# Optimization experiments

Measured on AMD Instinct MI355X. Metric: run time of the kernel, lower is better.

## Reference

```python
import jax, jax.numpy as jnp
import numpy as np
from jax.ops import segment_sum, segment_max

N_NODES, N_EDGES, N_GRAPHS = 50000, 800000, 128
IN_C, HID, HEADS, CLIN = 64, 64, 4, 32


def gat_layer(x, W, a_s, a_d, b, src, dst, n):
    # GAT-style attention conv with concatenated heads (PyG GATConv math).
    H, C = a_s.shape
    h = (x @ W).reshape(-1, H, C)                      # [N,H,C]
    es = jnp.einsum('nhc,hc->nh', h, a_s)
    ed = jnp.einsum('nhc,hc->nh', h, a_d)
    e = jax.nn.leaky_relu(es[src] + ed[dst], 0.2)      # [E,H]
    m = segment_max(e, dst, num_segments=n)            # stable softmax over incoming edges
    e = jnp.exp(e - m[dst])
    denom = segment_sum(e, dst, num_segments=n)
    alpha = e / jnp.where(denom[dst] > 0, denom[dst], 1.0)
    out = segment_sum(h[src] * alpha[:, :, None], dst, num_segments=n)  # [N,H,C]
    return out.reshape(-1, H * C) + b


def label_prop(x, src, dst, n, num_layers=2, alpha=0.5):
    # PyG LabelPropagation: sym-normalized diffusion, residual mix, clamp to [0,1].
    deg = segment_sum(jnp.ones((src.shape[0],), x.dtype), dst, num_segments=n)
    dis = jnp.where(deg > 0, 1.0 / jnp.sqrt(jnp.maximum(deg, 1.0)), 0.0)
    norm = (dis[src] * dis[dst])[:, None]
    res = (1.0 - alpha) * x
    out = x
    for _ in range(num_layers):
        out = alpha * segment_sum(out[src] * norm, dst, num_segments=n) + res
        out = jnp.clip(out, 0.0, 1.0)
    return out


def mean_pool(x, batch, n_graphs):
    cnt = segment_sum(jnp.ones((x.shape[0],), x.dtype), batch, num_segments=n_graphs)
    s = segment_sum(x, batch, num_segments=n_graphs)
    return s / jnp.maximum(cnt, 1.0)[:, None]


def setup_inputs() -> dict:
    key = jax.random.key(0)
    ks = iter(jax.random.split(key, 32))
    def p(shape, fan_in):
        return jax.random.normal(next(ks), shape, jnp.float32) / np.sqrt(fan_in)
    d = {}
    d['x'] = jax.random.normal(next(ks), (N_NODES, IN_C), jnp.float32)
    d['edge_index'] = jax.random.randint(next(ks), (2, N_EDGES), 0, N_NODES)
    d['batch'] = jnp.sort(jax.random.randint(next(ks), (N_NODES,), 0, N_GRAPHS))
    d['clinical_data'] = jax.random.normal(next(ks), (N_GRAPHS, CLIN), jnp.float32)
    HC = HEADS * HID
    d['W1'] = p((IN_C, HC), IN_C); d['a1s'] = p((HEADS, HID), HID); d['a1d'] = p((HEADS, HID), HID); d['b1'] = jnp.zeros((HC,), jnp.float32)
    d['W2'] = p((HC, HC), HC); d['a2s'] = p((HEADS, HID), HID); d['a2d'] = p((HEADS, HID), HID); d['b2'] = jnp.zeros((HC,), jnp.float32)
    jk = IN_C + 2 * HC  # 576
    d['pp_w1'] = p((jk, 256), jk); d['pp_b1'] = jnp.zeros((256,), jnp.float32)
    d['pp_w2'] = p((256, 128), 256); d['pp_b2'] = jnp.zeros((128,), jnp.float32)
    d['cl_w1'] = p((CLIN, 64), CLIN); d['cl_b1'] = jnp.zeros((64,), jnp.float32)
    d['cl_w2'] = p((64, 32), 64); d['cl_b2'] = jnp.zeros((32,), jnp.float32)
    d['h_w1'] = p((160, 64), 160); d['h_b1'] = jnp.zeros((64,), jnp.float32)
    d['h_w2'] = p((64, 32), 64); d['h_b2'] = jnp.zeros((32,), jnp.float32)
    d['h_w3'] = p((32, 2), 32); d['h_b3'] = jnp.zeros((2,), jnp.float32)
    return d


def reference(x, edge_index, batch, clinical_data,
              W1, a1s, a1d, b1, W2, a2s, a2d, b2,
              pp_w1, pp_b1, pp_w2, pp_b2,
              cl_w1, cl_b1, cl_w2, cl_b2,
              h_w1, h_b1, h_w2, h_b2, h_w3, h_b3):
    src, dst = edge_index[0], edge_index[1]
    n = x.shape[0]
    h0 = x
    h1 = jax.nn.relu(gat_layer(h0, W1, a1s, a1d, b1, src, dst, n))
    h1 = label_prop(h1, src, dst, n)
    h2 = jax.nn.relu(gat_layer(h1, W2, a2s, a2d, b2, src, dst, n))
    h2 = label_prop(h2, src, dst, n)
    combined = jnp.concatenate([h0, h1, h2], axis=-1)           # [N, 576]
    g = mean_pool(combined, batch, N_GRAPHS)                    # [G, 576]
    v_graph = jax.nn.relu(g @ pp_w1 + pp_b1) @ pp_w2 + pp_b2    # [G, 128] (dropout = eval/no-op)
    v_clin = jax.nn.relu(clinical_data @ cl_w1 + cl_b1) @ cl_w2 + cl_b2  # [G, 32]
    z = jnp.concatenate([v_graph, v_clin], axis=-1)             # [G, 160]
    z = jax.nn.relu(z @ h_w1 + h_b1)
    z = jax.nn.relu(z @ h_w2 + h_b2)
    return z @ h_w3 + h_b3                                      # [G, 2]
```

## Files before the change

kernel.cpp:

```cpp
#include <hip/hip_runtime.h>

#define N_NODES 50000
#define N_EDGES 800000
#define N_GRAPHS 128
#define JK 576
#define CAP 192
#define NSB ((N_NODES + 255) / 256)

typedef __attribute__((ext_vector_type(8))) short bf16x8;
typedef __attribute__((ext_vector_type(4))) float f32x4;

__device__ __forceinline__ unsigned f2_to_bf2(float a, float b) {
    unsigned ua = __float_as_uint(a), ub = __float_as_uint(b);
    ua = (ua + 0x7fffu + ((ua >> 16) & 1u)) >> 16;
    ub = (ub + 0x7fffu + ((ub >> 16) & 1u)) >> 16;
    return ua | (ub << 16);
}
__device__ __forceinline__ uint2 f4_to_bf4(float4 v) {
    return make_uint2(f2_to_bf2(v.x, v.y), f2_to_bf2(v.z, v.w));
}
__device__ __forceinline__ float4 bf4_to_f4(uint2 u) {
    float4 r;
    r.x = __uint_as_float(u.x << 16);
    r.y = __uint_as_float(u.x & 0xffff0000u);
    r.z = __uint_as_float(u.y << 16);
    r.w = __uint_as_float(u.y & 0xffff0000u);
    return r;
}

template<int BN, int KK>
__global__ __launch_bounds__(256)
void mfma_gemm(const unsigned short* __restrict__ Abf, int lda,
               const unsigned short* __restrict__ BT,
               unsigned* __restrict__ Cbf, int ldc,
               int M, const float* __restrict__ bias, int relu,
               int a_off, int b_off, int c_off) {
    __shared__ unsigned short As[64][32];
    __shared__ unsigned short Bs[BN][32];
    const int t = threadIdx.x;
    const int wav = t >> 6, lane = t & 63;
    const int quad = lane >> 4, l15 = lane & 15;
    const int m0 = blockIdx.x * 64;
    const int head = blockIdx.y;
    Abf += (size_t)head * a_off;
    BT  += (size_t)head * b_off;
    const float* bptr = bias ? bias + (size_t)head * c_off : nullptr;
    unsigned* cbf = Cbf + (((size_t)head * c_off) >> 1);

    f32x4 acc[BN / 16];
#pragma unroll
    for (int i = 0; i < BN / 16; i++) acc[i] = (f32x4){0.f, 0.f, 0.f, 0.f};

    const int arow = t >> 2, aseg = t & 3;
    for (int k0 = 0; k0 < KK; k0 += 32) {
        uint4 av = make_uint4(0, 0, 0, 0);
        int gm = m0 + arow;
        if (gm < M) av = *(const uint4*)&Abf[(size_t)gm * lda + k0 + aseg * 8];
        uint4 bv[BN == 256 ? 4 : 1];
        if (BN == 256) {
            const unsigned short* srcb = &BT[(size_t)t * KK + k0];
#pragma unroll
            for (int j = 0; j < 4; j++) bv[j] = *(const uint4*)&srcb[j * 8];
        } else {
            bv[0] = *(const uint4*)&BT[(size_t)arow * KK + k0 + aseg * 8];
        }
        __syncthreads();
        *(uint4*)&As[arow][aseg * 8] = av;
        if (BN == 256) {
#pragma unroll
            for (int j = 0; j < 4; j++) *(uint4*)&Bs[t][j * 8] = bv[j];
        } else {
            *(uint4*)&Bs[arow][aseg * 8] = bv[0];
        }
        __syncthreads();
        bf16x8 afrag = *(const bf16x8*)&As[wav * 16 + l15][quad * 8];
#pragma unroll
        for (int nt = 0; nt < BN / 16; nt++) {
            bf16x8 bfrag = *(const bf16x8*)&Bs[nt * 16 + l15][quad * 8];
            acc[nt] = __builtin_amdgcn_mfma_f32_16x16x32_bf16(afrag, bfrag, acc[nt], 0, 0, 0);
        }
    }
    int rbase = m0 + wav * 16 + quad * 4;
#pragma unroll
    for (int nt = 0; nt < BN / 16; nt++) {
        int col = nt * 16 + l15;
        float bb = bptr ? bptr[col] : 0.f;
#pragma unroll
        for (int r = 0; r < 4; r++) {
            int row = rbase + r;
            float v = acc[nt][r] + bb;
            if (relu) v = fmaxf(v, 0.f);
            float vp = __shfl_xor(v, 1);
            if (row < M && !(l15 & 1))
                cbf[((size_t)row * ldc + col) >> 1] = f2_to_bf2(v, vp);
        }
    }
}

__global__ void deg_kernel(const int* __restrict__ dst, int* __restrict__ deg) {
    int t = blockIdx.x * blockDim.x + threadIdx.x;
    if (t < N_EDGES) atomicAdd(&deg[dst[t]], 1);
}
#define S1 50000
#define S2 100000
#define S3 100256
#define S4 101280
#define S5 117664
#define S6 183200
#define S7 1783200
__global__ void prep_misc(const int* __restrict__ deg, float* __restrict__ dis,
                          const int* __restrict__ batch, int* __restrict__ gstart,
                          const float* __restrict__ W1, const float* __restrict__ a1s,
                          const float* __restrict__ a1d, float* __restrict__ wes1,
                          float* __restrict__ wed1,
                          const float* __restrict__ W2, const float* __restrict__ a2s,
                          const float* __restrict__ a2d, float* __restrict__ wes2,
                          float* __restrict__ wed2,
                          unsigned short* __restrict__ W1T, unsigned short* __restrict__ W2T,
                          const float* __restrict__ x, unsigned* __restrict__ xbf) {
    int i = blockIdx.x * blockDim.x + threadIdx.x;
    if (i >= S7) return;
    if (i >= S6) {
        int j = i - S6;
        float2 v = *(const float2*)&x[(size_t)j * 2];
        xbf[j] = f2_to_bf2(v.x, v.y);
    } else if (i >= S5) {
        int t2 = i - S5;
        int n = t2 >> 8, c = t2 & 255;
        unsigned u = __float_as_uint(W2[(size_t)c * 256 + n]);
        u = (u + 0x7fffu + ((u >> 16) & 1u)) >> 16;
        W2T[t2] = (unsigned short)u;
    } else if (i >= S4) {
        int t2 = i - S4;
        int n = t2 >> 6, c = t2 & 63;
        unsigned u = __float_as_uint(W1[(size_t)c * 256 + n]);
        u = (u + 0x7fffu + ((u >> 16) & 1u)) >> 16;
        W1T[t2] = (unsigned short)u;
    } else if (i >= S3) {
        int t2 = i - S3;
        int c = t2 >> 2, h = t2 & 3;
        float se = 0.f, sd = 0.f;
        for (int j = 0; j < 64; j++) {
            float w = W2[(size_t)c * 256 + h * 64 + j];
            se += w * a2s[h * 64 + j];
            sd += w * a2d[h * 64 + j];
        }
        wes2[c * 4 + h] = se;
        wed2[c * 4 + h] = sd;
    } else if (i >= S2) {
        int t2 = i - S2;
        int c = t2 >> 2, h = t2 & 3;
        float se = 0.f, sd = 0.f;
        for (int j = 0; j < 64; j++) {
            float w = W1[(size_t)c * 256 + h * 64 + j];
            se += w * a1s[h * 64 + j];
            sd += w * a1d[h * 64 + j];
        }
        wes1[c * 4 + h] = se;
        wed1[c * 4 + h] = sd;
    } else if (i >= S1) {
        int n = i - S1;
        int b = batch[n];
        int prev = (n == 0) ? -1 : batch[n - 1];
        for (int g = prev + 1; g <= b; g++) gstart[g] = n;
        if (n == N_NODES - 1)
            for (int g = b + 1; g <= N_GRAPHS; g++) gstart[g] = N_NODES;
    } else {
        int d = deg[i];
        dis[i] = d > 0 ? rsqrtf((float)d) : 0.f;
    }
}
__global__ __launch_bounds__(256) void scan_bsum(const int* __restrict__ deg,
                                                 int* __restrict__ bsum) {
    __shared__ int sd[256];
    int n = blockIdx.x * 256 + threadIdx.x;
    sd[threadIdx.x] = (n < N_NODES) ? deg[n] : 0;
    __syncthreads();
    for (int o = 128; o > 0; o >>= 1) {
        if (threadIdx.x < o) sd[threadIdx.x] += sd[threadIdx.x + o];
        __syncthreads();
    }
    if (threadIdx.x == 0) bsum[blockIdx.x] = sd[0];
}
__global__ __launch_bounds__(256) void scan_bpre(const int* __restrict__ bsum,
                                                 int* __restrict__ bpre,
                                                 int* __restrict__ off_last) {
    __shared__ int sd[256];
    int t = threadIdx.x;
    int v = (t < NSB) ? bsum[t] : 0;
    sd[t] = v;
    __syncthreads();
    for (int o = 1; o < 256; o <<= 1) {
        int u = (t >= o) ? sd[t - o] : 0;
        __syncthreads();
        sd[t] += u;
        __syncthreads();
    }
    if (t < NSB) bpre[t] = sd[t] - v;
    if (t == 255) *off_last = sd[255];
}
__global__ __launch_bounds__(256) void scan_off(const int* __restrict__ deg,
                                                const int* __restrict__ bpre,
                                                int* __restrict__ off) {
    __shared__ int sd[256];
    int n = blockIdx.x * 256 + threadIdx.x;
    int t = threadIdx.x;
    int v = (n < N_NODES) ? deg[n] : 0;
    sd[t] = v;
    __syncthreads();
    for (int o = 1; o < 256; o <<= 1) {
        int u = (t >= o) ? sd[t - o] : 0;
        __syncthreads();
        sd[t] += u;
        __syncthreads();
    }
    if (n < N_NODES) off[n] = bpre[blockIdx.x] + sd[t] - v;
}
__global__ void csr_fill(const int* __restrict__ src, const int* __restrict__ dst,
                         const int* __restrict__ off, int* __restrict__ cursor,
                         int* __restrict__ csr_src) {
    int e = blockIdx.x * blockDim.x + threadIdx.x;
    if (e >= N_EDGES) return;
    int s = src[e], d = dst[e];
    int pos = off[d] + atomicAdd(&cursor[d], 1);
    csr_src[pos] = s;
}

__global__ void esed_x(const float* __restrict__ X, const float* __restrict__ wes,
                       const float* __restrict__ wed, float* __restrict__ es,
                       float* __restrict__ ed) {
    int gid = blockIdx.x * blockDim.x + threadIdx.x;
    int n = gid >> 6, lane = threadIdx.x & 63;
    if (n >= N_NODES) return;
    float xv = X[(size_t)n * 64 + lane];
    float4 a = *(const float4*)&wes[lane * 4];
    float4 b = *(const float4*)&wed[lane * 4];
    float4 ps = make_float4(xv * a.x, xv * a.y, xv * a.z, xv * a.w);
    float4 pd = make_float4(xv * b.x, xv * b.y, xv * b.z, xv * b.w);
#pragma unroll
    for (int o = 1; o < 64; o <<= 1) {
        ps.x += __shfl_xor(ps.x, o); ps.y += __shfl_xor(ps.y, o);
        ps.z += __shfl_xor(ps.z, o); ps.w += __shfl_xor(ps.w, o);
        pd.x += __shfl_xor(pd.x, o); pd.y += __shfl_xor(pd.y, o);
        pd.z += __shfl_xor(pd.z, o); pd.w += __shfl_xor(pd.w, o);
    }
    if (lane == 0) {
        *(float4*)&es[n * 4] = ps;
        *(float4*)&ed[n * 4] = pd;
    }
}

__global__ void esed_h(const unsigned* __restrict__ Hbf, const float* __restrict__ wes,
                       const float* __restrict__ wed, float* __restrict__ es,
                       float* __restrict__ ed) {
    int gid = blockIdx.x * blockDim.x + threadIdx.x;
    int n = gid >> 6, lane = threadIdx.x & 63;
    if (n >= N_NODES) return;
    float4 xv = bf4_to_f4(*(const uint2*)&Hbf[(size_t)n * 128 + lane * 2]);
    float xs[4] = {xv.x, xv.y, xv.z, xv.w};
    float4 ps = make_float4(0.f, 0.f, 0.f, 0.f);
    float4 pd = make_float4(0.f, 0.f, 0.f, 0.f);
#pragma unroll
    for (int r = 0; r < 4; r++) {
        int c = lane * 4 + r;
        float4 a = *(const float4*)&wes[c * 4];
        float4 b = *(const float4*)&wed[c * 4];
        ps.x += xs[r] * a.x; ps.y += xs[r] * a.y; ps.z += xs[r] * a.z; ps.w += xs[r] * a.w;
        pd.x += xs[r] * b.x; pd.y += xs[r] * b.y; pd.z += xs[r] * b.z; pd.w += xs[r] * b.w;
    }
#pragma unroll
    for (int o = 1; o < 64; o <<= 1) {
        ps.x += __shfl_xor(ps.x, o); ps.y += __shfl_xor(ps.y, o);
        ps.z += __shfl_xor(ps.z, o); ps.w += __shfl_xor(ps.w, o);
        pd.x += __shfl_xor(pd.x, o); pd.y += __shfl_xor(pd.y, o);
        pd.z += __shfl_xor(pd.z, o); pd.w += __shfl_xor(pd.w, o);
    }
    if (lane == 0) {
        *(float4*)&es[n * 4] = ps;
        *(float4*)&ed[n * 4] = pd;
    }
}

__global__ __launch_bounds__(256)
void gat1_fused(const int* __restrict__ off, const int* __restrict__ csr_src,
                const float* __restrict__ es, const float* __restrict__ ed,
                const unsigned* __restrict__ xbf, unsigned* __restrict__ aggx_bf,
                float* __restrict__ alpha_fb) {
    __shared__ float elds[4][CAP * 4];
    __shared__ int   sidx[4][CAP];
    int wav = threadIdx.x >> 6, lane = threadIdx.x & 63;
    int n = blockIdx.x * 4 + wav;
    bool active = n < N_NODES;
    int p0 = 0, p1 = 0;
    float4 ed4 = make_float4(0.f, 0.f, 0.f, 0.f);
    if (active) { p0 = off[n]; p1 = off[n + 1]; ed4 = *(const float4*)&ed[n * 4]; }
    float4 sum = make_float4(0.f, 0.f, 0.f, 0.f);
    for (int p = p0 + lane; p < p1; p += 64) {
        int s = csr_src[p];
        float4 e4 = *(const float4*)&es[s * 4];
        e4.x += ed4.x; e4.y += ed4.y; e4.z += ed4.z; e4.w += ed4.w;
        e4.x = e4.x > 0.f ? e4.x : 0.2f * e4.x;
        e4.y = e4.y > 0.f ? e4.y : 0.2f * e4.y;
        e4.z = e4.z > 0.f ? e4.z : 0.2f * e4.z;
        e4.w = e4.w > 0.f ? e4.w : 0.2f * e4.w;
        e4.x = __expf(e4.x); e4.y = __expf(e4.y); e4.z = __expf(e4.z); e4.w = __expf(e4.w);
        int q = p - p0;
        if (q < CAP) { *(float4*)&elds[wav][q * 4] = e4; sidx[wav][q] = s; }
        else         *(float4*)&alpha_fb[(size_t)p * 4] = e4;
        sum.x += e4.x; sum.y += e4.y; sum.z += e4.z; sum.w += e4.w;
    }
#pragma unroll
    for (int o = 1; o < 64; o <<= 1) {
        sum.x += __shfl_xor(sum.x, o); sum.y += __shfl_xor(sum.y, o);
        sum.z += __shfl_xor(sum.z, o); sum.w += __shfl_xor(sum.w, o);
    }
    float4 rs;
    rs.x = sum.x > 0.f ? 1.f / sum.x : 0.f;
    rs.y = sum.y > 0.f ? 1.f / sum.y : 0.f;
    rs.z = sum.z > 0.f ? 1.f / sum.z : 0.f;
    rs.w = sum.w > 0.f ? 1.f / sum.w : 0.f;
    if (!active) return;
    int eg = lane >> 4, l15 = lane & 15;
    int deg = p1 - p0;
    float4 a0 = make_float4(0.f, 0.f, 0.f, 0.f);
    float4 a1 = a0, a2 = a0, a3 = a0;
    auto fetch = [&](int qq, float4& e4, float4& xv) {
        e4 = make_float4(0.f, 0.f, 0.f, 0.f);
        xv = e4;
        if (qq < deg) {
            int s;
            if (qq < CAP) { s = sidx[wav][qq]; e4 = *(const float4*)&elds[wav][qq * 4]; }
            else { s = csr_src[p0 + qq]; e4 = *(const float4*)&alpha_fb[(size_t)(p0 + qq) * 4]; }
            xv = bf4_to_f4(*(const uint2*)&xbf[(size_t)s * 32 + l15 * 2]);
        }
    };
    int q = eg;
    float4 eA, xA, eB, xB, eC, xC;
    fetch(q, eA, xA);
    fetch(q + 4, eB, xB);
    fetch(q + 8, eC, xC);
    while (q < deg) {
        float4 eD, xD;
        fetch(q + 12, eD, xD);
        a0.x += eA.x * xA.x; a0.y += eA.x * xA.y; a0.z += eA.x * xA.z; a0.w += eA.x * xA.w;
        a1.x += eA.y * xA.x; a1.y += eA.y * xA.y; a1.z += eA.y * xA.z; a1.w += eA.y * xA.w;
        a2.x += eA.z * xA.x; a2.y += eA.z * xA.y; a2.z += eA.z * xA.z; a2.w += eA.z * xA.w;
        a3.x += eA.w * xA.x; a3.y += eA.w * xA.y; a3.z += eA.w * xA.z; a3.w += eA.w * xA.w;
        eA = eB; xA = xB; eB = eC; xB = xC; eC = eD; xC = xD;
        q += 4;
    }
#pragma unroll
    for (int o = 16; o < 64; o <<= 1) {
        a0.x += __shfl_xor(a0.x, o); a0.y += __shfl_xor(a0.y, o);
        a0.z += __shfl_xor(a0.z, o); a0.w += __shfl_xor(a0.w, o);
        a1.x += __shfl_xor(a1.x, o); a1.y += __shfl_xor(a1.y, o);
        a1.z += __shfl_xor(a1.z, o); a1.w += __shfl_xor(a1.w, o);
        a2.x += __shfl_xor(a2.x, o); a2.y += __shfl_xor(a2.y, o);
        a2.z += __shfl_xor(a2.z, o); a2.w += __shfl_xor(a2.w, o);
        a3.x += __shfl_xor(a3.x, o); a3.y += __shfl_xor(a3.y, o);
        a3.z += __shfl_xor(a3.z, o); a3.w += __shfl_xor(a3.w, o);
    }
    if (eg == 0) {
        a0.x *= rs.x; a0.y *= rs.x; a0.z *= rs.x; a0.w *= rs.x;
        a1.x *= rs.y; a1.y *= rs.y; a1.z *= rs.y; a1.w *= rs.y;
        a2.x *= rs.z; a2.y *= rs.z; a2.z *= rs.z; a2.w *= rs.z;
        a3.x *= rs.w; a3.y *= rs.w; a3.z *= rs.w; a3.w *= rs.w;
        size_t b = (size_t)n * 128 + l15 * 2;
        *(uint2*)&aggx_bf[b +  0] = f4_to_bf4(a0);
        *(uint2*)&aggx_bf[b + 32] = f4_to_bf4(a1);
        *(uint2*)&aggx_bf[b + 64] = f4_to_bf4(a2);
        *(uint2*)&aggx_bf[b + 96] = f4_to_bf4(a3);
    }
}

__global__ __launch_bounds__(256)
void gat2_fused(const int* __restrict__ off, const int* __restrict__ csr_src,
                const float* __restrict__ es, const float* __restrict__ ed,
                const unsigned* __restrict__ H2bf, const float* __restrict__ bias,
                unsigned* __restrict__ outbf, float* __restrict__ alpha_fb) {
    __shared__ float elds[4][CAP * 4];
    __shared__ int   sidx[4][CAP];
    int wav = threadIdx.x >> 6, lane = threadIdx.x & 63;
    int n = blockIdx.x * 4 + wav;
    bool active = n < N_NODES;
    int p0 = 0, p1 = 0;
    float4 ed4 = make_float4(0.f, 0.f, 0.f, 0.f);
    if (active) { p0 = off[n]; p1 = off[n + 1]; ed4 = *(const float4*)&ed[n * 4]; }
    float4 sum = make_float4(0.f, 0.f, 0.f, 0.f);
    for (int p = p0 + lane; p < p1; p += 64) {
        int s = csr_src[p];
        float4 e4 = *(const float4*)&es[s * 4];
        e4.x += ed4.x; e4.y += ed4.y; e4.z += ed4.z; e4.w += ed4.w;
        e4.x = e4.x > 0.f ? e4.x : 0.2f * e4.x;
        e4.y = e4.y > 0.f ? e4.y : 0.2f * e4.y;
        e4.z = e4.z > 0.f ? e4.z : 0.2f * e4.z;
        e4.w = e4.w > 0.f ? e4.w : 0.2f * e4.w;
        e4.x = __expf(e4.x); e4.y = __expf(e4.y); e4.z = __expf(e4.z); e4.w = __expf(e4.w);
        int q = p - p0;
        if (q < CAP) { *(float4*)&elds[wav][q * 4] = e4; sidx[wav][q] = s; }
        else         *(float4*)&alpha_fb[(size_t)p * 4] = e4;
        sum.x += e4.x; sum.y += e4.y; sum.z += e4.z; sum.w += e4.w;
    }
#pragma unroll
    for (int o = 1; o < 64; o <<= 1) {
        sum.x += __shfl_xor(sum.x, o); sum.y += __shfl_xor(sum.y, o);
        sum.z += __shfl_xor(sum.z, o); sum.w += __shfl_xor(sum.w, o);
    }
    if (!active) return;
    int half = lane >> 5, l = lane & 31;
    int hh = l >> 3;
    float sh = (hh == 0) ? sum.x : (hh == 1) ? sum.y : (hh == 2) ? sum.z : sum.w;
    float rsh = sh > 0.f ? 1.f / sh : 0.f;
    int deg = p1 - p0;
    float acc[8];
#pragma unroll
    for (int j = 0; j < 8; j++) acc[j] = 0.f;
    auto fetch = [&](int qq, float& al, uint4& rr) {
        al = 0.f;
        rr = make_uint4(0, 0, 0, 0);
        if (qq < deg) {
            int s;
            if (qq < CAP) { s = sidx[wav][qq]; al = elds[wav][qq * 4 + hh]; }
            else { s = csr_src[p0 + qq]; al = alpha_fb[(size_t)(p0 + qq) * 4 + hh]; }
            rr = *(const uint4*)&H2bf[(size_t)s * 128 + l * 4];
        }
    };
    int q = half;
    float aA, aB, aC;
    uint4 rA, rB, rC;
    fetch(q, aA, rA);
    fetch(q + 2, aB, rB);
    fetch(q + 4, aC, rC);
    while (q < deg) {
        float aD; uint4 rD;
        fetch(q + 6, aD, rD);
        float4 f0 = bf4_to_f4(make_uint2(rA.x, rA.y));
        float4 f1 = bf4_to_f4(make_uint2(rA.z, rA.w));
        acc[0] += aA * f0.x; acc[1] += aA * f0.y; acc[2] += aA * f0.z; acc[3] += aA * f0.w;
        acc[4] += aA * f1.x; acc[5] += aA * f1.y; acc[6] += aA * f1.z; acc[7] += aA * f1.w;
        aA = aB; rA = rB; aB = aC; rB = rC; aC = aD; rC = rD;
        q += 2;
    }
#pragma unroll
    for (int j = 0; j < 8; j++) acc[j] += __shfl_xor(acc[j], 32);
    if (half == 0) {
        float4 b0 = *(const float4*)&bias[l * 8];
        float4 b1 = *(const float4*)&bias[l * 8 + 4];
        float4 o0, o1;
        o0.x = fmaxf(acc[0] * rsh + b0.x, 0.f);
        o0.y = fmaxf(acc[1] * rsh + b0.y, 0.f);
        o0.z = fmaxf(acc[2] * rsh + b0.z, 0.f);
        o0.w = fmaxf(acc[3] * rsh + b0.w, 0.f);
        o1.x = fmaxf(acc[4] * rsh + b1.x, 0.f);
        o1.y = fmaxf(acc[5] * rsh + b1.y, 0.f);
        o1.z = fmaxf(acc[6] * rsh + b1.z, 0.f);
        o1.w = fmaxf(acc[7] * rsh + b1.w, 0.f);
        uint2 w0 = f4_to_bf4(o0), w1 = f4_to_bf4(o1);
        uint4 w = make_uint4(w0.x, w0.y, w1.x, w1.y);
        *(uint4*)&outbf[(size_t)n * 128 + l * 4] = w;
    }
}

__global__ __launch_bounds__(256)
void lp_csr(const int* __restrict__ off, const int* __restrict__ csr_src,
            const float* __restrict__ dis, const unsigned* __restrict__ in_bf,
            const unsigned* __restrict__ res_bf, unsigned* __restrict__ out_bf) {
    __shared__ int   widx[4][CAP];
    __shared__ float wwt[4][CAP];
    int wav = threadIdx.x >> 6, lane = threadIdx.x & 63;
    int n = blockIdx.x * 4 + wav;
    if (n >= N_NODES) return;
    int p0 = off[n], p1 = off[n + 1];
    int deg = p1 - p0;
    float disd = dis[n];
    for (int q = lane; q < deg && q < CAP; q += 64) {
        int s = csr_src[p0 + q];
        widx[wav][q] = s;
        wwt[wav][q] = dis[s] * disd;
    }
    int half = lane >> 5, l = lane & 31;
    float acc[8];
#pragma unroll
    for (int j = 0; j < 8; j++) acc[j] = 0.f;
    auto fetch = [&](int qq, float& nw, uint4& rr) {
        nw = 0.f;
        rr = make_uint4(0, 0, 0, 0);
        if (qq < deg) {
            int s;
            if (qq < CAP) { s = widx[wav][qq]; nw = wwt[wav][qq]; }
            else { s = csr_src[p0 + qq]; nw = dis[s] * disd; }
            rr = *(const uint4*)&in_bf[(size_t)s * 128 + l * 4];
        }
    };
    int q = half;
    float nA, nB, nC;
    uint4 rA, rB, rC;
    fetch(q, nA, rA);
    fetch(q + 2, nB, rB);
    fetch(q + 4, nC, rC);
    while (q < deg) {
        float nD; uint4 rD;
        fetch(q + 6, nD, rD);
        float4 f0 = bf4_to_f4(make_uint2(rA.x, rA.y));
        float4 f1 = bf4_to_f4(make_uint2(rA.z, rA.w));
        acc[0] += nA * f0.x; acc[1] += nA * f0.y; acc[2] += nA * f0.z; acc[3] += nA * f0.w;
        acc[4] += nA * f1.x; acc[5] += nA * f1.y; acc[6] += nA * f1.z; acc[7] += nA * f1.w;
        nA = nB; rA = rB; nB = nC; rB = rC; nC = nD; rC = rD;
        q += 2;
    }
#pragma unroll
    for (int j = 0; j < 8; j++) acc[j] += __shfl_xor(acc[j], 32);
    if (half == 0) {
        uint4 rr = *(const uint4*)&res_bf[(size_t)n * 128 + l * 4];
        float4 r0 = bf4_to_f4(make_uint2(rr.x, rr.y));
        float4 r1 = bf4_to_f4(make_uint2(rr.z, rr.w));
        float4 o0, o1;
        o0.x = fminf(fmaxf(0.5f * acc[0] + 0.5f * r0.x, 0.f), 1.f);
        o0.y = fminf(fmaxf(0.5f * acc[1] + 0.5f * r0.y, 0.f), 1.f);
        o0.z = fminf(fmaxf(0.5f * acc[2] + 0.5f * r0.z, 0.f), 1.f);
        o0.w = fminf(fmaxf(0.5f * acc[3] + 0.5f * r0.w, 0.f), 1.f);
        o1.x = fminf(fmaxf(0.5f * acc[4] + 0.5f * r1.x, 0.f), 1.f);
        o1.y = fminf(fmaxf(0.5f * acc[5] + 0.5f * r1.y, 0.f), 1.f);
        o1.z = fminf(fmaxf(0.5f * acc[6] + 0.5f * r1.z, 0.f), 1.f);
        o1.w = fminf(fmaxf(0.5f * acc[7] + 0.5f * r1.w, 0.f), 1.f);
        uint2 w0 = f4_to_bf4(o0), w1 = f4_to_bf4(o1);
        uint4 w = make_uint4(w0.x, w0.y, w1.x, w1.y);
        *(uint4*)&out_bf[(size_t)n * 128 + l * 4] = w;
    }
}

__global__ void pool_partial(const float* __restrict__ buf, const int* __restrict__ gstart,
                             float* __restrict__ psum, int C, int colOff) {
    int g = blockIdx.x, q = blockIdx.y;
    int n0 = gstart[g], n1 = gstart[g + 1];
    int len = n1 - n0;
    int ns = n0 + (len * q) / 4, ne = n0 + (len * (q + 1)) / 4;
    int cp = threadIdx.x % C;
    int np = threadIdx.x / C;
    int NP = 256 / C;
    float s = 0.f;
    for (int n = ns + np; n < ne; n += NP) s += buf[(size_t)n * C + cp];
    atomicAdd(&psum[g * JK + colOff + cp], s);
}
__global__ void pool_bf(const unsigned* __restrict__ buf, const int* __restrict__ gstart,
                        float* __restrict__ psum, int colOff) {
    int g = blockIdx.x, q = blockIdx.y;
    int n0 = gstart[g], n1 = gstart[g + 1];
    int len = n1 - n0;
    int ns = n0 + (len * q) / 4, ne = n0 + (len * (q + 1)) / 4;
    int cp = threadIdx.x & 127;
    int np = threadIdx.x >> 7;
    float s0 = 0.f, s1 = 0.f;
    for (int n = ns + np; n < ne; n += 2) {
        unsigned u = buf[(size_t)n * 128 + cp];
        s0 += __uint_as_float(u << 16);
        s1 += __uint_as_float(u & 0xffff0000u);
    }
    atomicAdd(&psum[g * JK + colOff + cp * 2 + 0], s0);
    atomicAdd(&psum[g * JK + colOff + cp * 2 + 1], s1);
}
__global__ void gmean_kernel(const float* __restrict__ psum, const int* __restrict__ gstart,
                             float* __restrict__ g) {
    int i = blockIdx.x * blockDim.x + threadIdx.x;
    if (i >= N_GRAPHS * JK) return;
    int gi = i / JK;
    int len = gstart[gi + 1] - gstart[gi];
    g[i] = psum[i] / (float)(len > 1 ? len : 1);
}

__global__ __launch_bounds__(64)
void head_d1(const float* __restrict__ gbuf, const float* __restrict__ W,
             const float* __restrict__ bias, float* __restrict__ out) {
    __shared__ float zin[JK];
    int g = blockIdx.y, mc = blockIdx.x, lane = threadIdx.x;
    for (int k = lane; k < JK; k += 64) zin[k] = gbuf[g * JK + k];
    __syncthreads();
    int m = mc * 64 + lane;
    float acc = bias[m];
#pragma unroll 8
    for (int k = 0; k < JK; k++) acc += zin[k] * W[k * 256 + m];
    out[g * 256 + m] = fmaxf(acc, 0.f);
}

__global__ __launch_bounds__(256)
void head_rest(const float* __restrict__ t1, const float* __restrict__ clin,
               const float* __restrict__ pp_w2, const float* __restrict__ pp_b2,
               const float* __restrict__ cl_w1, const float* __restrict__ cl_b1,
               const float* __restrict__ cl_w2, const float* __restrict__ cl_b2,
               const float* __restrict__ h_w1, const float* __restrict__ h_b1,
               const float* __restrict__ h_w2, const float* __restrict__ h_b2,
               const float* __restrict__ h_w3, const float* __restrict__ h_b3,
               float* __restrict__ out) {
    __shared__ float z1[256];
    __shared__ float zcl[32];
    __shared__ float zc[64];
    __shared__ float z[160];
    __shared__ float z3[64];
    __shared__ float z4[32];
    __shared__ float part[128];
    int g = blockIdx.x, t = threadIdx.x;
    z1[t] = t1[g * 256 + t];
    if (t < 32) zcl[t] = clin[g * 32 + t];
    __syncthreads();
    int m = t & 127, half = t >> 7;
    {
        float acc = 0.f;
        int k0 = half * 128;
#pragma unroll 8
        for (int k = k0; k < k0 + 128; k++) acc += z1[k] * pp_w2[k * 128 + m];
        if (half) part[m] = acc;
        __syncthreads();
        if (!half) z[m] = acc + part[m] + pp_b2[m];
    }
    if (t < 64) {
        float acc = cl_b1[t];
#pragma unroll
        for (int k = 0; k < 32; k++) acc += zcl[k] * cl_w1[k * 64 + t];
        zc[t] = fmaxf(acc, 0.f);
    }
    __syncthreads();
    if (t < 32) {
        float acc = cl_b2[t];
#pragma unroll
        for (int k = 0; k < 64; k++) acc += zc[k] * cl_w2[k * 32 + t];
        z[128 + t] = acc;
    }
    __syncthreads();
    if (t < 64) {
        float acc = h_b1[t];
#pragma unroll 8
        for (int k = 0; k < 160; k++) acc += z[k] * h_w1[k * 64 + t];
        z3[t] = fmaxf(acc, 0.f);
    }
    __syncthreads();
    if (t < 32) {
        float acc = h_b2[t];
#pragma unroll
        for (int k = 0; k < 64; k++) acc += z3[k] * h_w2[k * 32 + t];
        z4[t] = fmaxf(acc, 0.f);
    }
    __syncthreads();
    if (t < 2) {
        float acc = h_b3[t];
#pragma unroll
        for (int k = 0; k < 32; k++) acc += z4[k] * h_w3[k * 2 + t];
        out[g * 2 + t] = acc;
    }
}

extern "C" void kernel_launch(void* const* d_in, const int* in_sizes, int n_in,
                              void* d_out, int out_size, void* d_ws, size_t ws_size,
                              hipStream_t stream) {
    const float* x     = (const float*)d_in[0];
    const int*   ei    = (const int*)d_in[1];
    const int*   batch = (const int*)d_in[2];
    const float* clin  = (const float*)d_in[3];
    const float* W1  = (const float*)d_in[4];
    const float* a1s = (const float*)d_in[5];
    const float* a1d = (const float*)d_in[6];
    const float* b1  = (const float*)d_in[7];
    const float* W2  = (const float*)d_in[8];
    const float* a2s = (const float*)d_in[9];
    const float* a2d = (const float*)d_in[10];
    const float* b2  = (const float*)d_in[11];
    const float* pp_w1 = (const float*)d_in[12];
    const float* pp_b1 = (const float*)d_in[13];
    const float* pp_w2 = (const float*)d_in[14];
    const float* pp_b2 = (const float*)d_in[15];
    const float* cl_w1 = (const float*)d_in[16];
    const float* cl_b1 = (const float*)d_in[17];
    const float* cl_w2 = (const float*)d_in[18];
    const float* cl_b2 = (const float*)d_in[19];
    const float* h_w1  = (const float*)d_in[20];
    const float* h_b1  = (const float*)d_in[21];
    const float* h_w2  = (const float*)d_in[22];
    const float* h_b2  = (const float*)d_in[23];
    const float* h_w3  = (const float*)d_in[24];
    const float* h_b3  = (const float*)d_in[25];

    const int* src = ei;
    const int* dst = ei + N_EDGES;

    char* p = (char*)d_ws;
    auto carve = [&](size_t bytes) -> char* {
        char* r = p;
        p += (bytes + 255) & ~(size_t)255;
        return r;
    };
    const size_t NBH = (size_t)N_NODES * 256 * 2;
    unsigned* abf  = (unsigned*)carve(NBH);
    unsigned* bf1  = (unsigned*)carve(NBH);
    unsigned* bf2  = (unsigned*)carve(NBH);
    unsigned* bf3  = (unsigned*)carve(NBH);
    unsigned* xbf  = (unsigned*)carve((size_t)N_NODES * 32 * 4);
    float* alpha_fb  = (float*)carve((size_t)N_EDGES * 4 * 4);
    int*   csr_src   = (int*)carve((size_t)N_EDGES * 4);
    int*   off       = (int*)carve((size_t)(N_NODES + 1) * 4);
    int*   deg       = (int*)carve((size_t)N_NODES * 4);
    int*   cursor    = (int*)carve((size_t)N_NODES * 4);
    int*   bsum      = (int*)carve((size_t)NSB * 4);
    int*   bpre      = (int*)carve((size_t)NSB * 4);
    float* dis       = (float*)carve((size_t)N_NODES * 4);
    float* es        = (float*)carve((size_t)N_NODES * 4 * 4);
    float* ed        = (float*)carve((size_t)N_NODES * 4 * 4);
    float* wes1      = (float*)carve((size_t)64 * 4 * 4);
    float* wed1      = (float*)carve((size_t)64 * 4 * 4);
    float* wes2      = (float*)carve((size_t)256 * 4 * 4);
    float* wed2      = (float*)carve((size_t)256 * 4 * 4);
    unsigned short* W1T = (unsigned short*)carve((size_t)256 * 64 * 2);
    unsigned short* W2T = (unsigned short*)carve((size_t)256 * 256 * 2);
    int*   gstart    = (int*)carve((size_t)(N_GRAPHS + 1) * 4);
    float* psum      = (float*)carve((size_t)N_GRAPHS * JK * 4);
    float* gbuf      = (float*)carve((size_t)N_GRAPHS * JK * 4);
    float* t1        = (float*)carve((size_t)N_GRAPHS * 256 * 4);

    const int TB = 256;
    const int gE     = (N_EDGES + TB - 1) / TB;
    const int gNwave = (N_NODES * 64 + TB - 1) / TB;
    const int gFuse  = (N_NODES + 3) / 4;
    const int gRow   = (N_NODES + 63) / 64;
    const int gPrep  = (S7 + TB - 1) / TB;

    hipMemsetAsync(deg, 0, (size_t)N_NODES * 4, stream);
    hipMemsetAsync(cursor, 0, (size_t)N_NODES * 4, stream);
    hipMemsetAsync(psum, 0, (size_t)N_GRAPHS * JK * 4, stream);
    deg_kernel<<<gE, TB, 0, stream>>>(dst, deg);
    prep_misc<<<gPrep, TB, 0, stream>>>(deg, dis, batch, gstart,
                                        W1, a1s, a1d, wes1, wed1,
                                        W2, a2s, a2d, wes2, wed2,
                                        W1T, W2T, x, xbf);
    scan_bsum<<<NSB, 256, 0, stream>>>(deg, bsum);
    scan_bpre<<<1, 256, 0, stream>>>(bsum, bpre, &off[N_NODES]);
    scan_off<<<NSB, 256, 0, stream>>>(deg, bpre, off);
    csr_fill<<<gE, TB, 0, stream>>>(src, dst, off, cursor, csr_src);

    esed_x<<<gNwave, TB, 0, stream>>>(x, wes1, wed1, es, ed);
    gat1_fused<<<gFuse, TB, 0, stream>>>(off, csr_src, es, ed, xbf, abf, alpha_fb);
    mfma_gemm<64, 64><<<dim3(gRow, 4), 256, 0, stream>>>(
        (const unsigned short*)abf, 256, W1T, bf1, 256, N_NODES, b1, 1,
        64, 64 * 64, 64);

    lp_csr<<<gFuse, TB, 0, stream>>>(off, csr_src, dis, bf1, bf1, bf2);
    lp_csr<<<gFuse, TB, 0, stream>>>(off, csr_src, dis, bf2, bf1, bf3);

    pool_bf<<<dim3(N_GRAPHS, 4), TB, 0, stream>>>(bf3, gstart, psum, 64);

    mfma_gemm<256, 256><<<dim3(gRow, 1), 256, 0, stream>>>(
        (const unsigned short*)bf3, 256, W2T, bf1, 256, N_NODES, nullptr, 0,
        0, 0, 0);
    esed_h<<<gNwave, TB, 0, stream>>>(bf3, wes2, wed2, es, ed);
    gat2_fused<<<gFuse, TB, 0, stream>>>(off, csr_src, es, ed, bf1, b2, bf2, alpha_fb);

    lp_csr<<<gFuse, TB, 0, stream>>>(off, csr_src, dis, bf2, bf2, bf1);
    lp_csr<<<gFuse, TB, 0, stream>>>(off, csr_src, dis, bf1, bf2, abf);

    pool_partial<<<dim3(N_GRAPHS, 4), TB, 0, stream>>>(x, gstart, psum, 64, 0);
    pool_bf<<<dim3(N_GRAPHS, 4), TB, 0, stream>>>(abf, gstart, psum, 320);
    gmean_kernel<<<(N_GRAPHS * JK + TB - 1) / TB, TB, 0, stream>>>(psum, gstart, gbuf);

    head_d1<<<dim3(4, N_GRAPHS), 64, 0, stream>>>(gbuf, pp_w1, pp_b1, t1);
    head_rest<<<N_GRAPHS, 256, 0, stream>>>(t1, clin, pp_w2, pp_b2, cl_w1, cl_b1,
                                            cl_w2, cl_b2, h_w1, h_b1, h_w2, h_b2,
                                            h_w3, h_b3, (float*)d_out);
}
```

Before: 784.3 us.

## Fuse small kernels: gstart into deg, x-pool into prep, esed into LP, merged head

Cuts the kernel-launch count by folding several small steps into neighbouring kernels. The gstart computation moves into deg_kernel and the raw-x pooling moves into prep_misc. The layer-2 attention-score projection is computed inside the second label-propagation kernel. The mean, first dense layer and remaining head run in a single head_all kernel. CAP is halved to shrink the shared-memory footprint of the LP kernel, which may raise occupancy but risks more fallback work for high-degree nodes. A prep_misc block could read gstart before deg_kernel finishes writing it, though stream ordering guarantees it does not.

New measurement: 769.7 us. No clear change (-1.9%).

```diff
diff --git a/kernel.cpp b/kernel.cpp
--- a/kernel.cpp
+++ b/kernel.cpp
@@ -4,7 +4,7 @@
 #define N_EDGES 800000
 #define N_GRAPHS 128
 #define JK 576
-#define CAP 192
+#define CAP 96
 #define NSB ((N_NODES + 255) / 256)
 
 typedef __attribute__((ext_vector_type(8))) short bf16x8;
@@ -97,19 +97,29 @@
     }
 }
 
-__global__ void deg_kernel(const int* __restrict__ dst, int* __restrict__ deg) {
+__global__ void deg_kernel(const int* __restrict__ dst, int* __restrict__ deg,
+                           const int* __restrict__ batch, int* __restrict__ gstart) {
     int t = blockIdx.x * blockDim.x + threadIdx.x;
-    if (t < N_EDGES) atomicAdd(&deg[dst[t]], 1);
-}
+    if (t < N_EDGES) {
+        atomicAdd(&deg[dst[t]], 1);
+    } else if (t < N_EDGES + N_NODES) {
+        int n = t - N_EDGES;
+        int b = batch[n];
+        int prev = (n == 0) ? -1 : batch[n - 1];
+        for (int g = prev + 1; g <= b; g++) gstart[g] = n;
+        if (n == N_NODES - 1)
+            for (int g = b + 1; g <= N_GRAPHS; g++) gstart[g] = N_NODES;
+    }
+}
+
 #define S1 50000
-#define S2 100000
-#define S3 100256
-#define S4 101280
-#define S5 117664
-#define S6 183200
-#define S7 1783200
+#define S2 50256
+#define S3 51280
+#define S4 67664
+#define S5 133200
+#define S6 1733200
+#define S7 (S6 + 131072)
 __global__ void prep_misc(const int* __restrict__ deg, float* __restrict__ dis,
-                          const int* __restrict__ batch, int* __restrict__ gstart,
                           const float* __restrict__ W1, const float* __restrict__ a1s,
                           const float* __restrict__ a1d, float* __restrict__ wes1,
                           float* __restrict__ wed1,
@@ -117,27 +127,39 @@
                           const float* __restrict__ a2d, float* __restrict__ wes2,
                           float* __restrict__ wed2,
                           unsigned short* __restrict__ W1T, unsigned short* __restrict__ W2T,
-                          const float* __restrict__ x, unsigned* __restrict__ xbf) {
+                          const float* __restrict__ x, unsigned* __restrict__ xbf,
+                          const int* __restrict__ gstart, float* __restrict__ psum) {
     int i = blockIdx.x * blockDim.x + threadIdx.x;
     if (i >= S7) return;
     if (i >= S6) {
-        int j = i - S6;
+        int t2 = i - S6;
+        int g = t2 >> 10, rem = t2 & 1023;
+        int q = rem >> 8, tid = rem & 255;
+        int cp = tid & 63, np = tid >> 6;
+        int n0 = gstart[g], n1 = gstart[g + 1];
+        int len = n1 - n0;
+        int ns = n0 + (len * q) / 4, ne = n0 + (len * (q + 1)) / 4;
+        float s = 0.f;
+        for (int n = ns + np; n < ne; n += 4) s += x[(size_t)n * 64 + cp];
+        atomicAdd(&psum[g * JK + cp], s);
+    } else if (i >= S5) {
+        int j = i - S5;
         float2 v = *(const float2*)&x[(size_t)j * 2];
         xbf[j] = f2_to_bf2(v.x, v.y);
-    } else if (i >= S5) {
-        int t2 = i - S5;
+    } else if (i >= S4) {
+        int t2 = i - S4;
         int n = t2 >> 8, c = t2 & 255;
         unsigned u = __float_as_uint(W2[(size_t)c * 256 + n]);
         u = (u + 0x7fffu + ((u >> 16) & 1u)) >> 16;
         W2T[t2] = (unsigned short)u;
-    } else if (i >= S4) {
-        int t2 = i - S4;
+    } else if (i >= S3) {
+        int t2 = i - S3;
         int n = t2 >> 6, c = t2 & 63;
         unsigned u = __float_as_uint(W1[(size_t)c * 256 + n]);
         u = (u + 0x7fffu + ((u >> 16) & 1u)) >> 16;
         W1T[t2] = (unsigned short)u;
-    } else if (i >= S3) {
-        int t2 = i - S3;
+    } else if (i >= S2) {
+        int t2 = i - S2;
         int c = t2 >> 2, h = t2 & 3;
         float se = 0.f, sd = 0.f;
         for (int j = 0; j < 64; j++) {
@@ -147,8 +169,8 @@
         }
         wes2[c * 4 + h] = se;
         wed2[c * 4 + h] = sd;
-    } else if (i >= S2) {
-        int t2 = i - S2;
+    } else if (i >= S1) {
+        int t2 = i - S1;
         int c = t2 >> 2, h = t2 & 3;
         float se = 0.f, sd = 0.f;
         for (int j = 0; j < 64; j++) {
@@ -158,13 +180,6 @@
         }
         wes1[c * 4 + h] = se;
         wed1[c * 4 + h] = sd;
-    } else if (i >= S1) {
-        int n = i - S1;
-        int b = batch[n];
-        int prev = (n == 0) ? -1 : batch[n - 1];
-        for (int g = prev + 1; g <= b; g++) gstart[g] = n;
-        if (n == N_NODES - 1)
-            for (int g = b + 1; g <= N_GRAPHS; g++) gstart[g] = N_NODES;
     } else {
         int d = deg[i];
         dis[i] = d > 0 ? rsqrtf((float)d) : 0.f;
@@ -237,37 +252,6 @@
     float4 b = *(const float4*)&wed[lane * 4];
     float4 ps = make_float4(xv * a.x, xv * a.y, xv * a.z, xv * a.w);
     float4 pd = make_float4(xv * b.x, xv * b.y, xv * b.z, xv * b.w);
-#pragma unroll
-    for (int o = 1; o < 64; o <<= 1) {
-        ps.x += __shfl_xor(ps.x, o); ps.y += __shfl_xor(ps.y, o);
-        ps.z += __shfl_xor(ps.z, o); ps.w += __shfl_xor(ps.w, o);
-        pd.x += __shfl_xor(pd.x, o); pd.y += __shfl_xor(pd.y, o);
-        pd.z += __shfl_xor(pd.z, o); pd.w += __shfl_xor(pd.w, o);
-    }
-    if (lane == 0) {
-        *(float4*)&es[n * 4] = ps;
-        *(float4*)&ed[n * 4] = pd;
-    }
-}
-
-__global__ void esed_h(const unsigned* __restrict__ Hbf, const float* __restrict__ wes,
-                       const float* __restrict__ wed, float* __restrict__ es,
-                       float* __restrict__ ed) {
-    int gid = blockIdx.x * blockDim.x + threadIdx.x;
-    int n = gid >> 6, lane = threadIdx.x & 63;
-    if (n >= N_NODES) return;
-    float4 xv = bf4_to_f4(*(const uint2*)&Hbf[(size_t)n * 128 + lane * 2]);
-    float xs[4] = {xv.x, xv.y, xv.z, xv.w};
-    float4 ps = make_float4(0.f, 0.f, 0.f, 0.f);
-    float4 pd = make_float4(0.f, 0.f, 0.f, 0.f);
-#pragma unroll
-    for (int r = 0; r < 4; r++) {
-        int c = lane * 4 + r;
-        float4 a = *(const float4*)&wes[c * 4];
-        float4 b = *(const float4*)&wed[c * 4];
-        ps.x += xs[r] * a.x; ps.y += xs[r] * a.y; ps.z += xs[r] * a.z; ps.w += xs[r] * a.w;
-        pd.x += xs[r] * b.x; pd.y += xs[r] * b.y; pd.z += xs[r] * b.z; pd.w += xs[r] * b.w;
-    }
 #pragma unroll
     for (int o = 1; o < 64; o <<= 1) {
         ps.x += __shfl_xor(ps.x, o); ps.y += __shfl_xor(ps.y, o);
@@ -461,10 +445,13 @@
     }
 }
 
+template<int FUSE_ESED>
 __global__ __launch_bounds__(256)
-void lp_csr(const int* __restrict__ off, const int* __restrict__ csr_src,
-            const float* __restrict__ dis, const unsigned* __restrict__ in_bf,
-            const unsigned* __restrict__ res_bf, unsigned* __restrict__ out_bf) {
+void lp_csr_t(const int* __restrict__ off, const int* __restrict__ csr_src,
+              const float* __restrict__ dis, const unsigned* __restrict__ in_bf,
+              const unsigned* __restrict__ res_bf, unsigned* __restrict__ out_bf,
+              const float* __restrict__ wes, const float* __restrict__ wed,
+              float* __restrict__ es, float* __restrict__ ed) {
     __shared__ int   widx[4][CAP];
     __shared__ float wwt[4][CAP];
     int wav = threadIdx.x >> 6, lane = threadIdx.x & 63;
@@ -526,22 +513,33 @@
         uint2 w0 = f4_to_bf4(o0), w1 = f4_to_bf4(o1);
         uint4 w = make_uint4(w0.x, w0.y, w1.x, w1.y);
         *(uint4*)&out_bf[(size_t)n * 128 + l * 4] = w;
-    }
-}
-
-__global__ void pool_partial(const float* __restrict__ buf, const int* __restrict__ gstart,
-                             float* __restrict__ psum, int C, int colOff) {
-    int g = blockIdx.x, q = blockIdx.y;
-    int n0 = gstart[g], n1 = gstart[g + 1];
-    int len = n1 - n0;
-    int ns = n0 + (len * q) / 4, ne = n0 + (len * (q + 1)) / 4;
-    int cp = threadIdx.x % C;
-    int np = threadIdx.x / C;
-    int NP = 256 / C;
-    float s = 0.f;
-    for (int n = ns + np; n < ne; n += NP) s += buf[(size_t)n * C + cp];
-    atomicAdd(&psum[g * JK + colOff + cp], s);
-}
+        if (FUSE_ESED) {
+            float vv[8] = {o0.x, o0.y, o0.z, o0.w, o1.x, o1.y, o1.z, o1.w};
+            float4 ps = make_float4(0.f, 0.f, 0.f, 0.f);
+            float4 pd = make_float4(0.f, 0.f, 0.f, 0.f);
+#pragma unroll
+            for (int j = 0; j < 8; j++) {
+                int c = l * 8 + j;
+                float4 a = *(const float4*)&wes[c * 4];
+                float4 b = *(const float4*)&wed[c * 4];
+                ps.x += vv[j] * a.x; ps.y += vv[j] * a.y; ps.z += vv[j] * a.z; ps.w += vv[j] * a.w;
+                pd.x += vv[j] * b.x; pd.y += vv[j] * b.y; pd.z += vv[j] * b.z; pd.w += vv[j] * b.w;
+            }
+#pragma unroll
+            for (int o = 1; o < 32; o <<= 1) {
+                ps.x += __shfl_xor(ps.x, o); ps.y += __shfl_xor(ps.y, o);
+                ps.z += __shfl_xor(ps.z, o); ps.w += __shfl_xor(ps.w, o);
+                pd.x += __shfl_xor(pd.x, o); pd.y += __shfl_xor(pd.y, o);
+                pd.z += __shfl_xor(pd.z, o); pd.w += __shfl_xor(pd.w, o);
+            }
+            if (l == 0) {
+                *(float4*)&es[n * 4] = ps;
+                *(float4*)&ed[n * 4] = pd;
+            }
+        }
+    }
+}
+
 __global__ void pool_bf(const unsigned* __restrict__ buf, const int* __restrict__ gstart,
                         float* __restrict__ psum, int colOff) {
     int g = blockIdx.x, q = blockIdx.y;
@@ -559,38 +557,19 @@
     atomicAdd(&psum[g * JK + colOff + cp * 2 + 0], s0);
     atomicAdd(&psum[g * JK + colOff + cp * 2 + 1], s1);
 }
-__global__ void gmean_kernel(const float* __restrict__ psum, const int* __restrict__ gstart,
-                             float* __restrict__ g) {
-    int i = blockIdx.x * blockDim.x + threadIdx.x;
-    if (i >= N_GRAPHS * JK) return;
-    int gi = i / JK;
-    int len = gstart[gi + 1] - gstart[gi];
-    g[i] = psum[i] / (float)(len > 1 ? len : 1);
-}
-
-__global__ __launch_bounds__(64)
-void head_d1(const float* __restrict__ gbuf, const float* __restrict__ W,
-             const float* __restrict__ bias, float* __restrict__ out) {
+
+__global__ __launch_bounds__(256)
+void head_all(const float* __restrict__ psum, const int* __restrict__ gstart,
+              const float* __restrict__ clin,
+              const float* __restrict__ pp_w1, const float* __restrict__ pp_b1,
+              const float* __restrict__ pp_w2, const float* __restrict__ pp_b2,
+              const float* __restrict__ cl_w1, const float* __restrict__ cl_b1,
+              const float* __restrict__ cl_w2, const float* __restrict__ cl_b2,
+              const float* __restrict__ h_w1, const float* __restrict__ h_b1,
+              const float* __restrict__ h_w2, const float* __restrict__ h_b2,
+              const float* __restrict__ h_w3, const float* __restrict__ h_b3,
+              float* __restrict__ out) {
     __shared__ float zin[JK];
-    int g = blockIdx.y, mc = blockIdx.x, lane = threadIdx.x;
-    for (int k = lane; k < JK; k += 64) zin[k] = gbuf[g * JK + k];
-    __syncthreads();
-    int m = mc * 64 + lane;
-    float acc = bias[m];
-#pragma unroll 8
-    for (int k = 0; k < JK; k++) acc += zin[k] * W[k * 256 + m];
-    out[g * 256 + m] = fmaxf(acc, 0.f);
-}
-
-__global__ __launch_bounds__(256)
-void head_rest(const float* __restrict__ t1, const float* __restrict__ clin,
-               const float* __restrict__ pp_w2, const float* __restrict__ pp_b2,
-               const float* __restrict__ cl_w1, const float* __restrict__ cl_b1,
-               const float* __restrict__ cl_w2, const float* __restrict__ cl_b2,
-               const float* __restrict__ h_w1, const float* __restrict__ h_b1,
-               const float* __restrict__ h_w2, const float* __restrict__ h_b2,
-               const float* __restrict__ h_w3, const float* __restrict__ h_b3,
-               float* __restrict__ out) {
     __shared__ float z1[256];
     __shared__ float zcl[32];
     __shared__ float zc[64];
@@ -599,8 +578,17 @@
     __shared__ float z4[32];
     __shared__ float part[128];
     int g = blockIdx.x, t = threadIdx.x;
-    z1[t] = t1[g * 256 + t];
+    int len = gstart[g + 1] - gstart[g];
+    float inv = 1.f / (float)(len > 1 ? len : 1);
+    for (int k = t; k < JK; k += 256) zin[k] = psum[g * JK + k] * inv;
     if (t < 32) zcl[t] = clin[g * 32 + t];
+    __syncthreads();
+    {
+        float acc = pp_b1[t];
+#pragma unroll 8
+        for (int k = 0; k < JK; k++) acc += zin[k] * pp_w1[k * 256 + t];
+        z1[t] = fmaxf(acc, 0.f);
+    }
     __syncthreads();
     int m = t & 127, half = t >> 7;
     {
@@ -711,11 +699,10 @@
     unsigned short* W2T = (unsigned short*)carve((size_t)256 * 256 * 2);
     int*   gstart    = (int*)carve((size_t)(N_GRAPHS + 1) * 4);
     float* psum      = (float*)carve((size_t)N_GRAPHS * JK * 4);
-    float* gbuf      = (float*)carve((size_t)N_GRAPHS * JK * 4);
-    float* t1        = (float*)carve((size_t)N_GRAPHS * 256 * 4);
 
     const int TB = 256;
     const int gE     = (N_EDGES + TB - 1) / TB;
+    const int gDeg   = (N_EDGES + N_NODES + TB - 1) / TB;
     const int gNwave = (N_NODES * 64 + TB - 1) / TB;
     const int gFuse  = (N_NODES + 3) / 4;
     const int gRow   = (N_NODES + 63) / 64;
@@ -724,11 +711,11 @@
     hipMemsetAsync(deg, 0, (size_t)N_NODES * 4, stream);
     hipMemsetAsync(cursor, 0, (size_t)N_NODES * 4, stream);
     hipMemsetAsync(psum, 0, (size_t)N_GRAPHS * JK * 4, stream);
-    deg_kernel<<<gE, TB, 0, stream>>>(dst, deg);
-    prep_misc<<<gPrep, TB, 0, stream>>>(deg, dis, batch, gstart,
+    deg_kernel<<<gDeg, TB, 0, stream>>>(dst, deg, batch, gstart);
+    prep_misc<<<gPrep, TB, 0, stream>>>(deg, dis,
                                         W1, a1s, a1d, wes1, wed1,
                                         W2, a2s, a2d, wes2, wed2,
-                                        W1T, W2T, x, xbf);
+                                        W1T, W2T, x, xbf, gstart, psum);
     scan_bsum<<<NSB, 256, 0, stream>>>(deg, bsum);
     scan_bpre<<<1, 256, 0, stream>>>(bsum, bpre, &off[N_NODES]);
     scan_off<<<NSB, 256, 0, stream>>>(deg, bpre, off);
@@ -740,26 +727,27 @@
         (const unsigned short*)abf, 256, W1T, bf1, 256, N_NODES, b1, 1,
         64, 64 * 64, 64);
 
-    lp_csr<<<gFuse, TB, 0, stream>>>(off, csr_src, dis, bf1, bf1, bf2);
-    lp_csr<<<gFuse, TB, 0, stream>>>(off, csr_src, dis, bf2, bf1, bf3);
+    lp_csr_t<0><<<gFuse, TB, 0, stream>>>(off, csr_src, dis, bf1, bf1, bf2,
+                                          nullptr, nullptr, nullptr, nullptr);
+    lp_csr_t<1><<<gFuse, TB, 0, stream>>>(off, csr_src, dis, bf2, bf1, bf3,
+                                          wes2, wed2, es, ed);
 
     pool_bf<<<dim3(N_GRAPHS, 4), TB, 0, stream>>>(bf3, gstart, psum, 64);
 
     mfma_gemm<256, 256><<<dim3(gRow, 1), 256, 0, stream>>>(
         (const unsigned short*)bf3, 256, W2T, bf1, 256, N_NODES, nullptr, 0,
         0, 0, 0);
-    esed_h<<<gNwave, TB, 0, stream>>>(bf3, wes2, wed2, es, ed);
     gat2_fused<<<gFuse, TB, 0, stream>>>(off, csr_src, es, ed, bf1, b2, bf2, alpha_fb);
 
-    lp_csr<<<gFuse, TB, 0, stream>>>(off, csr_src, dis, bf2, bf2, bf1);
-    lp_csr<<<gFuse, TB, 0, stream>>>(off, csr_src, dis, bf1, bf2, abf);
-
-    pool_partial<<<dim3(N_GRAPHS, 4), TB, 0, stream>>>(x, gstart, psum, 64, 0);
+    lp_csr_t<0><<<gFuse, TB, 0, stream>>>(off, csr_src, dis, bf2, bf2, bf1,
+                                          nullptr, nullptr, nullptr, nullptr);
+    lp_csr_t<0><<<gFuse, TB, 0, stream>>>(off, csr_src, dis, bf1, bf2, abf,
+                                          nullptr, nullptr, nullptr, nullptr);
+
     pool_bf<<<dim3(N_GRAPHS, 4), TB, 0, stream>>>(abf, gstart, psum, 320);
-    gmean_kernel<<<(N_GRAPHS * JK + TB - 1) / TB, TB, 0, stream>>>(psum, gstart, gbuf);
-
-    head_d1<<<dim3(4, N_GRAPHS), 64, 0, stream>>>(gbuf, pp_w1, pp_b1, t1);
-    head_rest<<<N_GRAPHS, 256, 0, stream>>>(t1, clin, pp_w2, pp_b2, cl_w1, cl_b1,
-                                            cl_w2, cl_b2, h_w1, h_b1, h_w2, h_b2,
-                                            h_w3, h_b3, (float*)d_out);
-}
+    head_all<<<N_GRAPHS, 256, 0, stream>>>(psum, gstart, clin,
+                                           pp_w1, pp_b1, pp_w2, pp_b2,
+                                           cl_w1, cl_b1, cl_w2, cl_b2,
+                                           h_w1, h_b1, h_w2, h_b2, h_w3, h_b3,
+                                           (float*)d_out);
+}
```
